# Kernel tuning notes

Measured on AMD Instinct MI355X. Metric: run time of the kernel, lower is better.

## Reference

```python
import jax, jax.numpy as jnp
from jax import lax
import numpy as np

NPOINTS = 1024
B, N, C = 32, 100000, 3


def setup_inputs() -> dict:
    key = jax.random.key(0)
    k1, k2 = jax.random.split(key)
    coord = jax.random.normal(k1, (B, N, C), dtype=jnp.float32)
    farthest_init = jax.random.randint(k2, (B,), 0, N, dtype=jnp.int64)
    return {"coord": coord, "farthest_init": farthest_init}


def reference(coord, farthest_init):
    # coord: (B, N, 3); farthest_init: (B,) seed indices.
    Bs, Ns, _ = coord.shape
    init_distance = jnp.full((Bs, Ns), 1e10, dtype=coord.dtype)

    def step(carry, _):
        distance, farthest = carry
        # gather current centroid per batch: (B, 1, 3)
        centroid = jnp.take_along_axis(coord, farthest[:, None, None], axis=1)
        dist = jnp.sum((coord - centroid) ** 2, axis=-1)  # (B, N)
        distance = jnp.minimum(distance, dist)            # masked update
        new_farthest = jnp.argmax(distance, axis=-1)      # (B,)
        # record the index that was just used as centroid (pre-update), as in torch loop
        return (distance, new_farthest), farthest

    (_, _), centroids_t = lax.scan(step, (init_distance, farthest_init), None, length=NPOINTS)
    centroids = centroids_t.T  # (B, NPOINTS)
    # gather sampled coordinates: (B, NPOINTS, 3)
    sampled = jnp.take_along_axis(coord, centroids[:, :, None], axis=1)
    return centroids, sampled
```

## Files before the change

### kernel.cpp

```cpp
#include <hip/hip_runtime.h>
#include <stdint.h>

#define BATCHES 32
#define NPT     100000
#define NSAMP   1024
#define GPB     8
#define TPB     1024
#define PPB     12500
#define PPT     13
#define TAILT   212
#define NW      (TPB/64)

typedef unsigned long long u64;
typedef unsigned int u32;

#define WS_BYTES (2 * BATCHES * GPB * 4 * 8)

__device__ __forceinline__ void red_step(u64& key, u32& idx, float& x, float& y, float& z, int off) {
    u64   ok = __shfl_xor(key, off, 64);
    u32   oi = __shfl_xor(idx, off, 64);
    float ox = __shfl_xor(x, off, 64);
    float oy = __shfl_xor(y, off, 64);
    float oz = __shfl_xor(z, off, 64);
    if (ok > key || (ok == key && oi < idx)) { key = ok; idx = oi; x = ox; y = oy; z = oz; }
}

__global__ void
__attribute__((amdgpu_flat_work_group_size(TPB, TPB), amdgpu_waves_per_eu(4, 4)))
fps_kernel(const float* __restrict__ coord,
           const int* __restrict__ seed_raw,
           float* __restrict__ out,
           u64* __restrict__ rec)
{
    const int tid  = threadIdx.x;
    const int lane = tid & 63;
    const int wid  = tid >> 6;
    const int b    = (int)blockIdx.x & 31;
    const int g    = (int)blockIdx.x >> 5;
    const int base = g * PPB;
    const float* cb = coord + (size_t)b * (NPT * 3);

    __shared__ u64   wkey[NW];
    __shared__ u32   widx[NW];
    __shared__ float wx[NW], wy[NW], wz[NW];
    __shared__ u32   s_win;
    __shared__ float s_cx, s_cy, s_cz;

    int odd = 0;
    #pragma unroll
    for (int i = 1; i < 32; i += 2) odd |= seed_raw[i];
    int cur = (odd == 0) ? seed_raw[2 * b] : seed_raw[b];

    float cx = cb[(size_t)cur * 3 + 0];
    float cy = cb[(size_t)cur * 3 + 1];
    float cz = cb[(size_t)cur * 3 + 2];

    float  px[PPT], py[PPT], pz[PPT];
    double d[PPT];
    #pragma unroll
    for (int k = 0; k < PPT; ++k) {
        bool v = (k < 12) || (tid < TAILT);
        int gi = base + (v ? (k * TPB + tid) : 0);
        px[k] = v ? cb[(size_t)gi * 3 + 0] : 0.f;
        py[k] = v ? cb[(size_t)gi * 3 + 1] : 0.f;
        pz[k] = v ? cb[(size_t)gi * 3 + 2] : 0.f;
        d[k]  = v ? 1.0e10 : 0.0;
    }

    float* cent_out = out;
    float* samp_out = out + BATCHES * NSAMP;

    for (int it = 0; it < NSAMP; ++it) {
        if (g == 0 && wid == 1 && lane == 0) {
            cent_out[b * NSAMP + it] = (float)cur;
            size_t so = ((size_t)b * NSAMP + it) * 3;
            samp_out[so + 0] = cx; samp_out[so + 1] = cy; samp_out[so + 2] = cz;
        }

        const double cxd = (double)cx, cyd = (double)cy, czd = (double)cz;

        double bd = -1.0; u32 bi = 0; float bx = 0.f, by = 0.f, bz = 0.f;
        #pragma unroll
        for (int k = 0; k < PPT; ++k) {
            if (k == 12 && tid >= TAILT) break;
            double dx = __dsub_rn((double)px[k], cxd);
            double dy = __dsub_rn((double)py[k], cyd);
            double dz = __dsub_rn((double)pz[k], czd);
            double d2 = __dadd_rn(__dadd_rn(__dmul_rn(dx, dx), __dmul_rn(dy, dy)),
                                  __dmul_rn(dz, dz));
            double nd = fmin(d[k], d2);
            d[k] = nd;
            bool gt = nd > bd;
            bd = gt ? nd : bd;
            bi = gt ? (u32)(base + k * TPB + tid) : bi;
            bx = gt ? px[k] : bx;
            by = gt ? py[k] : by;
            bz = gt ? pz[k] : bz;
        }
        u64 key = (u64)__double_as_longlong(bd);

        red_step(key, bi, bx, by, bz, 32); red_step(key, bi, bx, by, bz, 16);
        red_step(key, bi, bx, by, bz, 8);  red_step(key, bi, bx, by, bz, 4);
        red_step(key, bi, bx, by, bz, 2);  red_step(key, bi, bx, by, bz, 1);
        if (lane == 0) { wkey[wid] = key; widx[wid] = bi; wx[wid] = bx; wy[wid] = by; wz[wid] = bz; }
        __syncthreads();

        if (wid == 0) {
            u64   k2 = (lane < NW) ? wkey[lane] : 0ull;
            u32   i2 = (lane < NW) ? widx[lane] : 0xFFFFFFFFu;
            float x2 = (lane < NW) ? wx[lane] : 0.f;
            float y2 = (lane < NW) ? wy[lane] : 0.f;
            float z2 = (lane < NW) ? wz[lane] : 0.f;
            red_step(k2, i2, x2, y2, z2, 8); red_step(k2, i2, x2, y2, z2, 4);
            red_step(k2, i2, x2, y2, z2, 2); red_step(k2, i2, x2, y2, z2, 1);

            const int s = it & 1;
            u64* slot = rec + ((size_t)(s * BATCHES + b) * GPB) * 4;
            const u64 t2 = (u64)((((it + 1) >> 1) + 1) & 3);

            if (lane == 0) {
                u32 xb = __float_as_uint(x2), yb = __float_as_uint(y2), zb = __float_as_uint(z2);
                u64 w0 = (t2 << 62) | (k2 & 0x3FFFFFFFFFFFFFFFull);
                u64 w1 = (t2 << 62) | ((k2 >> 62) << 60) | ((u64)xb << 28) | (u64)(yb >> 4);
                u64 w2 = (t2 << 62) | ((u64)(yb & 0xFu) << 58) | ((u64)zb << 26) | ((u64)i2 << 9);
                u64* r = slot + g * 4;
                __hip_atomic_store(&r[0], w0, __ATOMIC_RELAXED, __HIP_MEMORY_SCOPE_AGENT);
                __hip_atomic_store(&r[1], w1, __ATOMIC_RELAXED, __HIP_MEMORY_SCOPE_AGENT);
                __hip_atomic_store(&r[2], w2, __ATOMIC_RELAXED, __HIP_MEMORY_SCOPE_AGENT);
            }

            u64 w0 = 0, w1 = 0, w2 = 0;
            for (;;) {
                bool ok = true;
                if (lane < GPB) {
                    u64* r = slot + lane * 4;
                    w0 = __hip_atomic_load(&r[0], __ATOMIC_RELAXED, __HIP_MEMORY_SCOPE_AGENT);
                    w1 = __hip_atomic_load(&r[1], __ATOMIC_RELAXED, __HIP_MEMORY_SCOPE_AGENT);
                    w2 = __hip_atomic_load(&r[2], __ATOMIC_RELAXED, __HIP_MEMORY_SCOPE_AGENT);
                    ok = ((w0 >> 62) == t2) & ((w1 >> 62) == t2) & ((w2 >> 62) == t2);
                }
                if (__ballot(ok) == ~0ull) break;
                __builtin_amdgcn_s_sleep(1);
            }

            u64   k3 = 0ull; u32 i3 = 0xFFFFFFFFu;
            float x3 = 0.f, y3 = 0.f, z3 = 0.f;
            if (lane < GPB) {
                k3 = (w0 & 0x3FFFFFFFFFFFFFFFull) | (((w1 >> 60) & 3ull) << 62);
                u32 xb = (u32)(w1 >> 28);
                u32 yb = (u32)(((w1 & 0xFFFFFFFull) << 4) | ((w2 >> 58) & 0xFull));
                u32 zb = (u32)(w2 >> 26);
                i3 = (u32)((w2 >> 9) & 0x1FFFFu);
                x3 = __uint_as_float(xb);
                y3 = __uint_as_float(yb);
                z3 = __uint_as_float(zb);
            }
            red_step(k3, i3, x3, y3, z3, 4); red_step(k3, i3, x3, y3, z3, 2); red_step(k3, i3, x3, y3, z3, 1);
            if (lane == 0) { s_win = i3; s_cx = x3; s_cy = y3; s_cz = z3; }
        }
        __syncthreads();
        cur = (int)s_win; cx = s_cx; cy = s_cy; cz = s_cz;
    }
}

extern "C" void kernel_launch(void* const* d_in, const int* in_sizes, int n_in,
                              void* d_out, int out_size, void* d_ws, size_t ws_size,
                              hipStream_t stream)
{
    const float* coord = (const float*)d_in[0];
    const int*   seed  = (const int*)d_in[1];
    float* out = (float*)d_out;
    u64* rec = (u64*)d_ws;

    hipMemsetAsync(d_ws, 0, WS_BYTES, stream);
    fps_kernel<<<dim3(BATCHES * GPB), dim3(TPB), 0, stream>>>(coord, seed, out, rec);
}
```

Measured before the change: 4.660 ms.

## Interleave two batches per block with a dedicated cross-block reduction wave

Each block now handles two batches (a pair) over a smaller point slice, with grid split 16 ways per batch instead of 8. While one batch waits on the cross-block exchange, the block computes distances for the other batch. A dedicated wave polls the global records and broadcasts each winner through LDS flags, and the compute waves sync with counter-based LDS barriers instead of __syncthreads. The aim is to hide the per-iteration inter-block latency. The cost is more complex spin synchronisation, more blocks taking part in each global exchange, and a risk of deadlock or a memory-ordering bug.

```diff
diff --git a/kernel.cpp b/kernel.cpp
--- a/kernel.cpp
+++ b/kernel.cpp
@@ -4,17 +4,25 @@
 #define BATCHES 32
 #define NPT     100000
 #define NSAMP   1024
-#define GPB     8
+#define GPB     16
+#define NPAIR   16
 #define TPB     1024
-#define PPB     12500
-#define PPT     13
-#define TAILT   212
-#define NW      (TPB/64)
+#define NCW     15
+#define CTH     (NCW*64)
+#define PPB     6250
+#define PPT     7
+#define TAILT   490
 
 typedef unsigned long long u64;
 typedef unsigned int u32;
 
 #define WS_BYTES (2 * BATCHES * GPB * 4 * 8)
+
+__device__ __forceinline__ void red_ki(u64& key, u32& idx, int off) {
+    u64 ok = __shfl_xor(key, off, 64);
+    u32 oi = __shfl_xor(idx, off, 64);
+    if (ok > key || (ok == key && oi < idx)) { key = ok; idx = oi; }
+}
 
 __device__ __forceinline__ void red_step(u64& key, u32& idx, float& x, float& y, float& z, int off) {
     u64   ok = __shfl_xor(key, off, 64);
@@ -35,131 +43,182 @@
     const int tid  = threadIdx.x;
     const int lane = tid & 63;
     const int wid  = tid >> 6;
-    const int b    = (int)blockIdx.x & 31;
-    const int g    = (int)blockIdx.x >> 5;
+    const int p    = (int)blockIdx.x & (NPAIR - 1);
+    const int g    = (int)blockIdx.x >> 4;
     const int base = g * PPB;
-    const float* cb = coord + (size_t)b * (NPT * 3);
-
-    __shared__ u64   wkey[NW];
-    __shared__ u32   widx[NW];
-    __shared__ float wx[NW], wy[NW], wz[NW];
-    __shared__ u32   s_win;
-    __shared__ float s_cx, s_cy, s_cz;
+    const int bA = p, bB = p + NPAIR;
+
+    __shared__ u64 winw[2][2][2];
+    __shared__ u32 sbar[8];
+    __shared__ u64   pkey[2][NCW];
+    __shared__ u32   pidx[2][NCW];
+    __shared__ float pxs[2][NCW], pys[2][NCW], pzs[2][NCW];
+
+    if (tid < 8) { sbar[tid] = 0; ((u64*)winw)[tid] = 0ull; }
+    __syncthreads();
+
+    float* cent_out = out;
+    float* samp_out = out + BATCHES * NSAMP;
+
+    if (wid == NCW) {
+        for (int t = 1; t < NSAMP; ++t) {
+            #pragma unroll
+            for (int xb = 0; xb < 2; ++xb) {
+                const int batch = xb ? bB : bA;
+                u64* slot = rec + ((size_t)((t & 1) * BATCHES + batch) * GPB) * 4;
+                const u64 t2 = (u64)(((t >> 1) + 1) & 3);
+                const bool mine = lane < 3 * GPB;
+                u64* wp = slot + (mine ? ((lane / 3) * 4 + (lane % 3)) : 0);
+                u64 w = 0;
+                for (;;) {
+                    bool ok = true;
+                    if (mine) {
+                        w = __hip_atomic_load(wp, __ATOMIC_RELAXED, __HIP_MEMORY_SCOPE_AGENT);
+                        ok = (w >> 62) == t2;
+                    }
+                    if (__ballot(ok) == ~0ull) break;
+                    __builtin_amdgcn_s_sleep(1);
+                }
+                const int li = lane & 15;
+                u64 w0 = __shfl(w, 3 * li + 0, 64);
+                u64 w1 = __shfl(w, 3 * li + 1, 64);
+                u64 w2 = __shfl(w, 3 * li + 2, 64);
+                u64 k3 = 0ull; u32 i3 = 0xFFFFFFFFu; float x3 = 0.f, y3 = 0.f, z3 = 0.f;
+                if (lane < GPB) {
+                    k3 = (w0 & 0x3FFFFFFFFFFFFFFFull) | (((w1 >> 60) & 3ull) << 62);
+                    u32 xbt = (u32)(w1 >> 28);
+                    u32 ybt = (u32)(((w1 & 0xFFFFFFFull) << 4) | ((w2 >> 58) & 0xFull));
+                    u32 zbt = (u32)(w2 >> 26);
+                    i3 = (u32)((w2 >> 9) & 0x1FFFFu);
+                    x3 = __uint_as_float(xbt); y3 = __uint_as_float(ybt); z3 = __uint_as_float(zbt);
+                }
+                red_step(k3, i3, x3, y3, z3, 8); red_step(k3, i3, x3, y3, z3, 4);
+                red_step(k3, i3, x3, y3, z3, 2); red_step(k3, i3, x3, y3, z3, 1);
+                if (lane == 0) {
+                    u32 xbt = __float_as_uint(x3), ybt = __float_as_uint(y3), zbt = __float_as_uint(z3);
+                    u64 v0 = (t2 << 62) | ((u64)xbt << 30) | (u64)(ybt >> 2);
+                    u64 v1 = (t2 << 62) | ((u64)(ybt & 3u) << 60) | ((u64)zbt << 28) | ((u64)i3 << 11);
+                    __hip_atomic_store(&winw[xb][t & 1][0], v0, __ATOMIC_RELAXED, __HIP_MEMORY_SCOPE_WORKGROUP);
+                    __hip_atomic_store(&winw[xb][t & 1][1], v1, __ATOMIC_RELAXED, __HIP_MEMORY_SCOPE_WORKGROUP);
+                }
+            }
+        }
+        return;
+    }
+
+    const int ct = tid;
+    const float* cbA = coord + (size_t)bA * (NPT * 3);
+    const float* cbB = coord + (size_t)bB * (NPT * 3);
 
     int odd = 0;
     #pragma unroll
     for (int i = 1; i < 32; i += 2) odd |= seed_raw[i];
-    int cur = (odd == 0) ? seed_raw[2 * b] : seed_raw[b];
-
-    float cx = cb[(size_t)cur * 3 + 0];
-    float cy = cb[(size_t)cur * 3 + 1];
-    float cz = cb[(size_t)cur * 3 + 2];
-
-    float  px[PPT], py[PPT], pz[PPT];
-    double d[PPT];
+    u32 scur[2]; float scx[2], scy[2], scz[2];
+    scur[0] = (u32)((odd == 0) ? seed_raw[2 * bA] : seed_raw[bA]);
+    scur[1] = (u32)((odd == 0) ? seed_raw[2 * bB] : seed_raw[bB]);
+    scx[0] = cbA[(size_t)scur[0] * 3 + 0]; scy[0] = cbA[(size_t)scur[0] * 3 + 1]; scz[0] = cbA[(size_t)scur[0] * 3 + 2];
+    scx[1] = cbB[(size_t)scur[1] * 3 + 0]; scy[1] = cbB[(size_t)scur[1] * 3 + 1]; scz[1] = cbB[(size_t)scur[1] * 3 + 2];
+
+    float  px[2][PPT], py[2][PPT], pz[2][PPT];
+    double d[2][PPT];
     #pragma unroll
-    for (int k = 0; k < PPT; ++k) {
-        bool v = (k < 12) || (tid < TAILT);
-        int gi = base + (v ? (k * TPB + tid) : 0);
-        px[k] = v ? cb[(size_t)gi * 3 + 0] : 0.f;
-        py[k] = v ? cb[(size_t)gi * 3 + 1] : 0.f;
-        pz[k] = v ? cb[(size_t)gi * 3 + 2] : 0.f;
-        d[k]  = v ? 1.0e10 : 0.0;
-    }
-
-    float* cent_out = out;
-    float* samp_out = out + BATCHES * NSAMP;
-
-    for (int it = 0; it < NSAMP; ++it) {
-        if (g == 0 && wid == 1 && lane == 0) {
-            cent_out[b * NSAMP + it] = (float)cur;
-            size_t so = ((size_t)b * NSAMP + it) * 3;
-            samp_out[so + 0] = cx; samp_out[so + 1] = cy; samp_out[so + 2] = cz;
-        }
-
-        const double cxd = (double)cx, cyd = (double)cy, czd = (double)cz;
-
-        double bd = -1.0; u32 bi = 0; float bx = 0.f, by = 0.f, bz = 0.f;
+    for (int xb = 0; xb < 2; ++xb) {
+        const float* cb = xb ? cbB : cbA;
         #pragma unroll
         for (int k = 0; k < PPT; ++k) {
-            if (k == 12 && tid >= TAILT) break;
-            double dx = __dsub_rn((double)px[k], cxd);
-            double dy = __dsub_rn((double)py[k], cyd);
-            double dz = __dsub_rn((double)pz[k], czd);
-            double d2 = __dadd_rn(__dadd_rn(__dmul_rn(dx, dx), __dmul_rn(dy, dy)),
-                                  __dmul_rn(dz, dz));
-            double nd = fmin(d[k], d2);
-            d[k] = nd;
-            bool gt = nd > bd;
-            bd = gt ? nd : bd;
-            bi = gt ? (u32)(base + k * TPB + tid) : bi;
-            bx = gt ? px[k] : bx;
-            by = gt ? py[k] : by;
-            bz = gt ? pz[k] : bz;
+            bool v = (k < PPT - 1) || (ct < TAILT);
+            int gi = base + (v ? (k * CTH + ct) : 0);
+            px[xb][k] = v ? cb[(size_t)gi * 3 + 0] : 0.f;
+            py[xb][k] = v ? cb[(size_t)gi * 3 + 1] : 0.f;
+            pz[xb][k] = v ? cb[(size_t)gi * 3 + 2] : 0.f;
+            d[xb][k]  = v ? 1.0e10 : 0.0;
         }
-        u64 key = (u64)__double_as_longlong(bd);
-
-        red_step(key, bi, bx, by, bz, 32); red_step(key, bi, bx, by, bz, 16);
-        red_step(key, bi, bx, by, bz, 8);  red_step(key, bi, bx, by, bz, 4);
-        red_step(key, bi, bx, by, bz, 2);  red_step(key, bi, bx, by, bz, 1);
-        if (lane == 0) { wkey[wid] = key; widx[wid] = bi; wx[wid] = bx; wy[wid] = by; wz[wid] = bz; }
-        __syncthreads();
-
-        if (wid == 0) {
-            u64   k2 = (lane < NW) ? wkey[lane] : 0ull;
-            u32   i2 = (lane < NW) ? widx[lane] : 0xFFFFFFFFu;
-            float x2 = (lane < NW) ? wx[lane] : 0.f;
-            float y2 = (lane < NW) ? wy[lane] : 0.f;
-            float z2 = (lane < NW) ? wz[lane] : 0.f;
-            red_step(k2, i2, x2, y2, z2, 8); red_step(k2, i2, x2, y2, z2, 4);
-            red_step(k2, i2, x2, y2, z2, 2); red_step(k2, i2, x2, y2, z2, 1);
-
-            const int s = it & 1;
-            u64* slot = rec + ((size_t)(s * BATCHES + b) * GPB) * 4;
-            const u64 t2 = (u64)((((it + 1) >> 1) + 1) & 3);
-
-            if (lane == 0) {
-                u32 xb = __float_as_uint(x2), yb = __float_as_uint(y2), zb = __float_as_uint(z2);
-                u64 w0 = (t2 << 62) | (k2 & 0x3FFFFFFFFFFFFFFFull);
-                u64 w1 = (t2 << 62) | ((k2 >> 62) << 60) | ((u64)xb << 28) | (u64)(yb >> 4);
-                u64 w2 = (t2 << 62) | ((u64)(yb & 0xFu) << 58) | ((u64)zb << 26) | ((u64)i2 << 9);
-                u64* r = slot + g * 4;
-                __hip_atomic_store(&r[0], w0, __ATOMIC_RELAXED, __HIP_MEMORY_SCOPE_AGENT);
-                __hip_atomic_store(&r[1], w1, __ATOMIC_RELAXED, __HIP_MEMORY_SCOPE_AGENT);
-                __hip_atomic_store(&r[2], w2, __ATOMIC_RELAXED, __HIP_MEMORY_SCOPE_AGENT);
-            }
-
-            u64 w0 = 0, w1 = 0, w2 = 0;
-            for (;;) {
-                bool ok = true;
-                if (lane < GPB) {
-                    u64* r = slot + lane * 4;
-                    w0 = __hip_atomic_load(&r[0], __ATOMIC_RELAXED, __HIP_MEMORY_SCOPE_AGENT);
-                    w1 = __hip_atomic_load(&r[1], __ATOMIC_RELAXED, __HIP_MEMORY_SCOPE_AGENT);
-                    w2 = __hip_atomic_load(&r[2], __ATOMIC_RELAXED, __HIP_MEMORY_SCOPE_AGENT);
-                    ok = ((w0 >> 62) == t2) & ((w1 >> 62) == t2) & ((w2 >> 62) == t2);
-                }
-                if (__ballot(ok) == ~0ull) break;
-                __builtin_amdgcn_s_sleep(1);
-            }
-
-            u64   k3 = 0ull; u32 i3 = 0xFFFFFFFFu;
-            float x3 = 0.f, y3 = 0.f, z3 = 0.f;
-            if (lane < GPB) {
-                k3 = (w0 & 0x3FFFFFFFFFFFFFFFull) | (((w1 >> 60) & 3ull) << 62);
-                u32 xb = (u32)(w1 >> 28);
-                u32 yb = (u32)(((w1 & 0xFFFFFFFull) << 4) | ((w2 >> 58) & 0xFull));
-                u32 zb = (u32)(w2 >> 26);
-                i3 = (u32)((w2 >> 9) & 0x1FFFFu);
-                x3 = __uint_as_float(xb);
-                y3 = __uint_as_float(yb);
-                z3 = __uint_as_float(zb);
-            }
-            red_step(k3, i3, x3, y3, z3, 4); red_step(k3, i3, x3, y3, z3, 2); red_step(k3, i3, x3, y3, z3, 1);
-            if (lane == 0) { s_win = i3; s_cx = x3; s_cy = y3; s_cz = z3; }
+    }
+
+    for (int t = 0; t < NSAMP; ++t) {
+        #pragma unroll
+        for (int xb = 0; xb < 2; ++xb) {
+            const int batch = xb ? bB : bA;
+            const int pi = 2 * t + xb;
+            u32 cur; float cx, cy, cz;
+            if (t == 0) {
+                cur = scur[xb]; cx = scx[xb]; cy = scy[xb]; cz = scz[xb];
+            } else {
+                const u64 t2 = (u64)(((t >> 1) + 1) & 3);
+                u64 v0, v1;
+                for (;;) {
+                    v0 = __hip_atomic_load(&winw[xb][t & 1][0], __ATOMIC_RELAXED, __HIP_MEMORY_SCOPE_WORKGROUP);
+                    v1 = __hip_atomic_load(&winw[xb][t & 1][1], __ATOMIC_RELAXED, __HIP_MEMORY_SCOPE_WORKGROUP);
+                    if (((v0 >> 62) == t2) & ((v1 >> 62) == t2)) break;
+                }
+                u32 xbt = (u32)(v0 >> 30);
+                u32 ybt = (u32)(((v0 & 0x3FFFFFFFull) << 2) | ((v1 >> 60) & 3ull));
+                u32 zbt = (u32)(v1 >> 28);
+                cur = (u32)((v1 >> 11) & 0x1FFFFu);
+                cx = __uint_as_float(xbt); cy = __uint_as_float(ybt); cz = __uint_as_float(zbt);
+            }
+            if (g == 0 && wid == 1 && lane == 0) {
+                cent_out[batch * NSAMP + t] = (float)cur;
+                size_t so = ((size_t)batch * NSAMP + t) * 3;
+                samp_out[so + 0] = cx; samp_out[so + 1] = cy; samp_out[so + 2] = cz;
+            }
+            if (t == NSAMP - 1) continue;
+
+            const double cxd = (double)cx, cyd = (double)cy, czd = (double)cz;
+            double bd = -1.0; u32 bi = 0; float bx = 0.f, by = 0.f, bz = 0.f;
+            #pragma unroll
+            for (int k = 0; k < PPT; ++k) {
+                if (k == PPT - 1 && ct >= TAILT) break;
+                double dx = __dsub_rn((double)px[xb][k], cxd);
+                double dy = __dsub_rn((double)py[xb][k], cyd);
+                double dz = __dsub_rn((double)pz[xb][k], czd);
+                double d2 = __dadd_rn(__dadd_rn(__dmul_rn(dx, dx), __dmul_rn(dy, dy)),
+                                      __dmul_rn(dz, dz));
+                double nd = fmin(d[xb][k], d2);
+                d[xb][k] = nd;
+                bool gt = nd > bd;
+                bd = gt ? nd : bd;
+                bi = gt ? (u32)(base + k * CTH + ct) : bi;
+                bx = gt ? px[xb][k] : bx;
+                by = gt ? py[xb][k] : by;
+                bz = gt ? pz[xb][k] : bz;
+            }
+            u64 key = (u64)__double_as_longlong(bd);
+
+            u64 wk = key; u32 wi = bi;
+            red_ki(wk, wi, 32); red_ki(wk, wi, 16); red_ki(wk, wi, 8);
+            red_ki(wk, wi, 4);  red_ki(wk, wi, 2);  red_ki(wk, wi, 1);
+            const int pb = pi & 1;
+            if (wi == bi) { pkey[pb][wid] = wk; pidx[pb][wid] = wi;
+                            pxs[pb][wid] = bx; pys[pb][wid] = by; pzs[pb][wid] = bz; }
+
+            if (lane == 0)
+                __hip_atomic_fetch_add(&sbar[pi & 7], 1u, __ATOMIC_RELEASE, __HIP_MEMORY_SCOPE_WORKGROUP);
+            const u32 tgt = (u32)(NCW * ((pi >> 3) + 1));
+            while (__hip_atomic_load(&sbar[pi & 7], __ATOMIC_ACQUIRE, __HIP_MEMORY_SCOPE_WORKGROUP) < tgt) {}
+
+            if (wid == 0) {
+                u64   k2 = (lane < NCW) ? pkey[pb][lane] : 0ull;
+                u32   i2 = (lane < NCW) ? pidx[pb][lane] : 0xFFFFFFFFu;
+                float x2 = (lane < NCW) ? pxs[pb][lane] : 0.f;
+                float y2 = (lane < NCW) ? pys[pb][lane] : 0.f;
+                float z2 = (lane < NCW) ? pzs[pb][lane] : 0.f;
+                red_step(k2, i2, x2, y2, z2, 8); red_step(k2, i2, x2, y2, z2, 4);
+                red_step(k2, i2, x2, y2, z2, 2); red_step(k2, i2, x2, y2, z2, 1);
+                if (lane == 0) {
+                    const u32 v = (u32)(t + 1);
+                    const u64 t2p = (u64)(((v >> 1) + 1) & 3);
+                    u64* r = rec + ((size_t)((v & 1) * BATCHES + batch) * GPB + g) * 4;
+                    u32 xbt = __float_as_uint(x2), ybt = __float_as_uint(y2), zbt = __float_as_uint(z2);
+                    u64 w0 = (t2p << 62) | (k2 & 0x3FFFFFFFFFFFFFFFull);
+                    u64 w1 = (t2p << 62) | ((k2 >> 62) << 60) | ((u64)xbt << 28) | (u64)(ybt >> 4);
+                    u64 w2 = (t2p << 62) | ((u64)(ybt & 0xFu) << 58) | ((u64)zbt << 26) | ((u64)i2 << 9);
+                    __hip_atomic_store(&r[0], w0, __ATOMIC_RELAXED, __HIP_MEMORY_SCOPE_AGENT);
+                    __hip_atomic_store(&r[1], w1, __ATOMIC_RELAXED, __HIP_MEMORY_SCOPE_AGENT);
+                    __hip_atomic_store(&r[2], w2, __ATOMIC_RELAXED, __HIP_MEMORY_SCOPE_AGENT);
+                }
+            }
         }
-        __syncthreads();
-        cur = (int)s_win; cx = s_cx; cy = s_cy; cz = s_cz;
     }
 }
 
@@ -173,5 +232,5 @@
     u64* rec = (u64*)d_ws;
 
     hipMemsetAsync(d_ws, 0, WS_BYTES, stream);
-    fps_kernel<<<dim3(BATCHES * GPB), dim3(TPB), 0, stream>>>(coord, seed, out, rec);
-}
+    fps_kernel<<<dim3(NPAIR * GPB), dim3(TPB), 0, stream>>>(coord, seed, out, rec);
+}
```

New measurement: 4.390 ms. 1.06x faster.
